# Kernel tuning notes

Measured on AMD Instinct MI355X. Metric: run time of the kernel, lower is better.

## Reference

```python
import jax, jax.numpy as jnp
import numpy as np

B, N, C, NH = 8, 16384, 256, 8
CH = C // NH          # head dim = 32
SCALE = CH ** -0.5
HH = WW = 128         # N = HH*WW
# CoaT crpe window dict {3:2, 5:3, 7:3}: 2 heads->3x3, 3 heads->5x5, 3 heads->7x7


def setup_inputs() -> dict:
    key = jax.random.key(0)
    ks = jax.random.split(key, 9)
    w = lambda k, shp: (jax.random.normal(k, shp, jnp.float32) * 0.02)
    return {
        "x": jax.random.normal(ks[0], (B, N, C), jnp.float32),
        "w_qkv": w(ks[1], (C, 3 * C)),              # qkv_bias=False
        "w_proj": w(ks[2], (C, C)),
        "b_proj": jnp.zeros((C,), jnp.float32),
        "w3": w(ks[3], (3, 3, 1, 2 * CH)),          # HWIO depthwise, 2 heads
        "b3": jnp.zeros((2 * CH,), jnp.float32),
        "w5": w(ks[4], (5, 5, 1, 3 * CH)),          # 3 heads
        "b5": jnp.zeros((3 * CH,), jnp.float32),
        "w7": w(ks[5], (7, 7, 1, 3 * CH)),          # 3 heads
        "b7": jnp.zeros((3 * CH,), jnp.float32),
        "H": HH,
        "W": WW,
    }


def _hydra(q, k, v):
    # q,k,v: [B, h, N, Ch]; normalize over feature dim, O(N) token reduction
    qn = q * jax.lax.rsqrt(jnp.sum(q * q, axis=-1, keepdims=True))
    kn = k * jax.lax.rsqrt(jnp.sum(k * k, axis=-1, keepdims=True))
    kv = jnp.sum(kn * v, axis=-2, keepdims=True)   # [B, h, 1, Ch]
    return qn * kv                                  # broadcast over tokens


def _dwconv(img, kern, bias):
    # img: [B, c, H, W]; kern: [kh, kw, 1, c] (HWIO depthwise)
    c = img.shape[1]
    out = jax.lax.conv_general_dilated(
        img, kern, window_strides=(1, 1), padding="SAME",
        feature_group_count=c,
        dimension_numbers=("NCHW", "HWIO", "NCHW"))
    return out + bias[None, :, None, None]


def _crpe(q, v, Hs, Ws, convs):
    # CoaT ConvRelPosEnc: depthwise conv on v per head group, gated by q
    b, h, n, ch = v.shape
    outs, idx = [], 0
    for heads, kern, bias in convs:
        vs = v[:, idx:idx + heads]                          # [B, hs, N, Ch]
        v_img = vs.transpose(0, 1, 3, 2).reshape(b, heads * ch, Hs, Ws)
        cv = _dwconv(v_img, kern, bias)
        cv = cv.reshape(b, heads, ch, n).transpose(0, 1, 3, 2)
        outs.append(q[:, idx:idx + heads] * cv)
        idx += heads
    return jnp.concatenate(outs, axis=1)                    # [B, h, N, Ch]


def reference(x, w_qkv, w_proj, b_proj, w3, b3, w5, b5, w7, b7, H, W):
    b, n, c = x.shape
    qkv = (x @ w_qkv).reshape(b, n, 3, NH, CH).transpose(2, 0, 3, 1, 4)
    q, k, v = qkv[0], qkv[1], qkv[2]                        # [B, h, N, Ch]
    factor_att = _hydra(q, k, v)
    crpe = _crpe(q, v, H, W, [(2, w3, b3), (3, w5, b5), (3, w7, b7)])
    out = SCALE * factor_att + crpe
    out = out.transpose(0, 2, 1, 3).reshape(b, n, c)        # [B, N, C]
    return out @ w_proj + b_proj
```

## Files before the change

### kernel.cpp

```cpp
#include <hip/hip_runtime.h>
#include <hip/hip_bf16.h>


typedef __hip_bfloat16 bf16;
typedef __bf16 bf16x8 __attribute__((ext_vector_type(8)));
typedef unsigned short u16x8 __attribute__((ext_vector_type(8)));
typedef float f32x4 __attribute__((ext_vector_type(4)));
typedef float f32x8 __attribute__((ext_vector_type(8)));

#define SCALE_ 0.17677669529663687f

__device__ __forceinline__ unsigned short f2b(float f) {
  __hip_bfloat16 h = __float2bfloat16(f);
  return __builtin_bit_cast(unsigned short, h);
}
__device__ __forceinline__ float blo(unsigned u) {
  return __builtin_bit_cast(float, u << 16);
}
__device__ __forceinline__ float bhi(unsigned u) {
  return __builtin_bit_cast(float, u & 0xffff0000u);
}
__device__ __forceinline__ f32x8 unpack8(uint4 u) {
  f32x8 r;
  r[0] = blo(u.x); r[1] = bhi(u.x); r[2] = blo(u.y); r[3] = bhi(u.y);
  r[4] = blo(u.z); r[5] = bhi(u.z); r[6] = blo(u.w); r[7] = bhi(u.w);
  return r;
}
__device__ __forceinline__ uint4 pack8(float a0, float a1, float a2, float a3,
                                       float a4, float a5, float a6, float a7) {
  uint4 s;
  s.x = (unsigned)f2b(a0) | ((unsigned)f2b(a1) << 16);
  s.y = (unsigned)f2b(a2) | ((unsigned)f2b(a3) << 16);
  s.z = (unsigned)f2b(a4) | ((unsigned)f2b(a5) << 16);
  s.w = (unsigned)f2b(a6) | ((unsigned)f2b(a7) << 16);
  return s;
}
__device__ __forceinline__ void gload16(const void* g, void* l) {
  __builtin_amdgcn_global_load_lds(
      (const __attribute__((address_space(1))) unsigned int*)g,
      (__attribute__((address_space(3))) unsigned int*)l, 16, 0, 0);
}
__device__ __forceinline__ f32x4 mfma16(u16x8 a, u16x8 b, f32x4 c) {
  return __builtin_amdgcn_mfma_f32_16x16x32_bf16(
      __builtin_bit_cast(bf16x8, a), __builtin_bit_cast(bf16x8, b), c, 0, 0, 0);
}
__device__ __forceinline__ void barrier_vm4() {
  asm volatile("s_waitcnt vmcnt(4) lgkmcnt(0)" ::: "memory");
  __builtin_amdgcn_s_barrier();
  asm volatile("" ::: "memory");
}
__device__ __forceinline__ void barrier_vm0() {
  asm volatile("s_waitcnt vmcnt(0) lgkmcnt(0)" ::: "memory");
  __builtin_amdgcn_s_barrier();
  asm volatile("" ::: "memory");
}
__device__ __forceinline__ void barrier_vm8() {
  asm volatile("s_waitcnt vmcnt(8) lgkmcnt(0)" ::: "memory");
  __builtin_amdgcn_s_barrier();
  asm volatile("" ::: "memory");
}

__global__ __launch_bounds__(256) void prep_weights(
    const float* __restrict__ wqkv, const float* __restrict__ wproj,
    bf16* __restrict__ wqkvT, bf16* __restrict__ wprojT) {
  const int idx = blockIdx.x * 256 + threadIdx.x;
  if (idx < 768 * 256) {
    const int j = idx >> 8, k = idx & 255;
    wqkvT[idx] = __float2bfloat16(wqkv[k * 768 + j]);
  }
  if (idx < 256 * 256) {
    const int j = idx >> 8, k = idx & 255;
    wprojT[idx] = __float2bfloat16(wproj[k * 256 + j]);
  }
}

__global__ __launch_bounds__(256) void qkv_mfma(
    const float* __restrict__ x, const bf16* __restrict__ wT,
    bf16* __restrict__ qO, bf16* __restrict__ kO, bf16* __restrict__ vO) {
  __shared__ __align__(16) char LDSU[32768];
  char* As = LDSU;
  char* Bs = LDSU + 16384;
  const int tid = threadIdx.x;
  const int l = tid & 63, w = tid >> 6;
  const int wr = w >> 1, wc = w & 1;

  const int lin = blockIdx.y * 6 + blockIdx.x;
  const int xcd = lin & 7, qq = lin >> 3;
  const int jt = qq % 6;
  const int ttile = xcd * 128 + qq / 6;
  const int j0 = jt << 7;
  const int t0 = ttile << 7;

  f32x4 acc[4][4];
#pragma unroll
  for (int m = 0; m < 4; ++m)
#pragma unroll
    for (int t = 0; t < 4; ++t) acc[m][t] = (f32x4){0.f, 0.f, 0.f, 0.f};

  const int arow0 = w * 16 + (l >> 2), arow1 = arow0 + 64;
  const int asl = l & 3;
  const bf16* asrc0 =
      wT + (size_t)(j0 + arow0) * 256 + ((asl ^ ((arow0 >> 1) & 3)) << 3);
  const bf16* asrc1 =
      wT + (size_t)(j0 + arow1) * 256 + ((asl ^ ((arow1 >> 1) & 3)) << 3);
  const int ad0 = w * 1024, ad1 = 4096 + w * 1024;

  const int brow = tid >> 1, bkh = tid & 1;
  const float* xp = x + (size_t)(t0 + brow) * 256 + bkh * 16;
  const int bsw = (brow >> 1) & 3;
  const int bw0 = brow * 64 + (((bkh << 1) ^ bsw) << 4);
  const int bw1 = brow * 64 + ((((bkh << 1) | 1) ^ bsw) << 4);

  const int fr = l & 15;
  const int fq = l >> 4;
  const int fs = (fq ^ ((l >> 1) & 3)) << 4;

  float4 xs[3][4];

  gload16(asrc0, As + ad0);
  gload16(asrc1, As + ad1);
#pragma unroll
  for (int s = 0; s < 3; ++s)
#pragma unroll
    for (int i = 0; i < 4; ++i)
      xs[s][i] = *(const float4*)(xp + s * 32 + i * 4);
  {
    u16x8 p0, p1;
    p0[0] = f2b(xs[0][0].x); p0[1] = f2b(xs[0][0].y);
    p0[2] = f2b(xs[0][0].z); p0[3] = f2b(xs[0][0].w);
    p0[4] = f2b(xs[0][1].x); p0[5] = f2b(xs[0][1].y);
    p0[6] = f2b(xs[0][1].z); p0[7] = f2b(xs[0][1].w);
    p1[0] = f2b(xs[0][2].x); p1[1] = f2b(xs[0][2].y);
    p1[2] = f2b(xs[0][2].z); p1[3] = f2b(xs[0][2].w);
    p1[4] = f2b(xs[0][3].x); p1[5] = f2b(xs[0][3].y);
    p1[6] = f2b(xs[0][3].z); p1[7] = f2b(xs[0][3].w);
    *(u16x8*)(Bs + bw0) = p0;
    *(u16x8*)(Bs + bw1) = p1;
  }
  barrier_vm8();

#pragma unroll
  for (int t = 0; t < 8; ++t) {
    if (t < 7) {
      const int kn = (t + 1) << 5;
      char* Adst = As + (((t + 1) & 1) << 13);
      gload16(asrc0 + kn, Adst + ad0);
      gload16(asrc1 + kn, Adst + ad1);
    }
    if (t < 5) {
#pragma unroll
      for (int i = 0; i < 4; ++i)
        xs[t % 3][i] = *(const float4*)(xp + (t + 3) * 32 + i * 4);
    }
    const char* Ac = As + ((t & 1) << 13);
    const char* Bc = Bs + ((t & 1) << 13);
    u16x8 af[4], bfv[4];
#pragma unroll
    for (int m = 0; m < 4; ++m)
      af[m] = *(const u16x8*)(Ac + (wr * 64 + m * 16 + fr) * 64 + fs);
#pragma unroll
    for (int tt = 0; tt < 4; ++tt)
      bfv[tt] = *(const u16x8*)(Bc + (wc * 64 + tt * 16 + fr) * 64 + fs);
    __builtin_amdgcn_s_setprio(1);
#pragma unroll
    for (int m = 0; m < 4; ++m)
#pragma unroll
      for (int tt = 0; tt < 4; ++tt)
        acc[m][tt] = mfma16(af[m], bfv[tt], acc[m][tt]);
    __builtin_amdgcn_s_setprio(0);
    if (t < 7) {
      const float4* xv = xs[(t + 1) % 3];
      u16x8 p0, p1;
      p0[0] = f2b(xv[0].x); p0[1] = f2b(xv[0].y);
      p0[2] = f2b(xv[0].z); p0[3] = f2b(xv[0].w);
      p0[4] = f2b(xv[1].x); p0[5] = f2b(xv[1].y);
      p0[6] = f2b(xv[1].z); p0[7] = f2b(xv[1].w);
      p1[0] = f2b(xv[2].x); p1[1] = f2b(xv[2].y);
      p1[2] = f2b(xv[2].z); p1[3] = f2b(xv[2].w);
      p1[4] = f2b(xv[3].x); p1[5] = f2b(xv[3].y);
      p1[6] = f2b(xv[3].z); p1[7] = f2b(xv[3].w);
      char* Bdst = Bs + (((t + 1) & 1) << 13);
      *(u16x8*)(Bdst + bw0) = p0;
      *(u16x8*)(Bdst + bw1) = p1;
    }
    if (t < 5) barrier_vm4();
    else if (t < 7) barrier_vm0();
  }
  __syncthreads();

#pragma unroll
  for (int m = 0; m < 4; ++m) {
    const int jq = wr * 16 + m * 4 + fq;
#pragma unroll
    for (int t = 0; t < 4; ++t) {
      const int token = wc * 64 + t * 16 + fr;
      const int p = jq ^ (token & 15);
      uint2 pk;
      pk.x = (unsigned)f2b(acc[m][t][0]) | ((unsigned)f2b(acc[m][t][1]) << 16);
      pk.y = (unsigned)f2b(acc[m][t][2]) | ((unsigned)f2b(acc[m][t][3]) << 16);
      *(uint2*)(LDSU + token * 256 + (p << 3)) = pk;
    }
  }
  __syncthreads();

  const int region = j0 >> 8;
  bf16* outp = (region == 0) ? qO : ((region == 1) ? kO : vO);
  const int b = t0 >> 14;
  const int n0 = t0 & 16383;
  const int jl = j0 & 255;
  const int seg = tid & 15;
#pragma unroll
  for (int r = 0; r < 8; ++r) {
    const int token = r * 16 + (tid >> 4);
    const int tsw = token & 15;
    const uint2 lo = *(const uint2*)(LDSU + token * 256 + (((2 * seg) ^ tsw) << 3));
    const uint2 hi =
        *(const uint2*)(LDSU + token * 256 + (((2 * seg + 1) ^ tsw) << 3));
    uint4 d;
    d.x = lo.x; d.y = lo.y; d.z = hi.x; d.w = hi.y;
    *(uint4*)&outp[((size_t)b * 16384 + n0 + token) * 256 + jl + seg * 8] = d;
  }
}

__global__ __launch_bounds__(256) void kv_reduce(
    const bf16* __restrict__ kT, const bf16* __restrict__ vT,
    float* __restrict__ kv) {
  __shared__ float red[256 * 8];
  const int tid = threadIdx.x;
  const int b = blockIdx.y;
  const int seg = tid & 31;
  f32x8 part = (f32x8)0.f;

  for (int r = 0; r < 32; ++r) {
    const int token = blockIdx.x * 256 + r * 8 + (tid >> 5);
    const size_t roff = ((size_t)b * 16384 + token) * 256;
    const uint4 kd = *(const uint4*)(kT + roff + seg * 8);
    const f32x8 kf = unpack8(kd);
    float ss = 0.f;
#pragma unroll
    for (int i = 0; i < 8; ++i) ss += kf[i] * kf[i];
    ss += __shfl_xor(ss, 1);
    ss += __shfl_xor(ss, 2);
    const float inv = rsqrtf(ss);
    const uint4 vd = *(const uint4*)(vT + roff + seg * 8);
    const f32x8 vf = unpack8(vd);
#pragma unroll
    for (int i = 0; i < 8; ++i) part[i] += kf[i] * inv * vf[i];
  }
#pragma unroll
  for (int i = 0; i < 8; ++i) red[tid * 8 + i] = part[i];
  __syncthreads();
  if (tid < 32) {
    f32x8 s = (f32x8)0.f;
#pragma unroll
    for (int k = 0; k < 8; ++k)
#pragma unroll
      for (int i = 0; i < 8; ++i) s[i] += red[(tid + 32 * k) * 8 + i];
#pragma unroll
    for (int i = 0; i < 8; ++i)
      atomicAdd(&kv[b * 256 + seg * 8 + i], s[i]);
  }
}

#define CRPE_SMEM 37632

template <int K>
__device__ __forceinline__ void crpe_impl(
    char* smem, const bf16* __restrict__ qT, const bf16* __restrict__ vT,
    const float* __restrict__ kvbuf, const float* __restrict__ wp,
    const float* __restrict__ bp, int OC, int hg, int h,
    bf16* __restrict__ mid) {
  constexpr int R = K / 2;
  constexpr int S = 16 + 2 * R;
  constexpr int NSLOT = 4 * ((S - 1) * 23 + 1);
  char* vs = smem;
  float* wlds = (float*)(smem + NSLOT * 16);
  float* blds = wlds + K * K * 32;

  const int tid = threadIdx.x;
  const int tile = blockIdx.y;
  const int b = blockIdx.z;
  const int tx0 = (tile & 7) * 16, ty0 = (tile >> 3) * 16;
  const int px = tid & 15, py = tid >> 4;
  const int ocbase = hg * 32;

  for (int e = tid; e < S * S; e += 256) {
    const int ly = e / S, lx = e - ly * S;
    const int gy = ty0 - R + ly, gx = tx0 - R + lx;
    uint4 d0 = {0, 0, 0, 0}, d1 = {0, 0, 0, 0}, d2 = {0, 0, 0, 0},
          d3 = {0, 0, 0, 0};
    if (gy >= 0 && gy < 128 && gx >= 0 && gx < 128) {
      const uint4* src = (const uint4*)(vT +
          ((size_t)b * 16384 + gy * 128 + gx) * 256 + h * 32);
      d0 = src[0]; d1 = src[1]; d2 = src[2]; d3 = src[3];
    }
    const int p = ly * 22 + lx;
    const int sw = (p >> 1) & 3;
    char* base = vs + ((p << 2) << 4);
    *(uint4*)(base + ((0 ^ sw) << 4)) = d0;
    *(uint4*)(base + ((1 ^ sw) << 4)) = d1;
    *(uint4*)(base + ((2 ^ sw) << 4)) = d2;
    *(uint4*)(base + ((3 ^ sw) << 4)) = d3;
  }
  for (int e = tid; e < K * K * 32; e += 256)
    wlds[e] = wp[(e >> 5) * OC + ocbase + (e & 31)];
  if (tid < 32) blds[tid] = bp[ocbase + tid];
  __syncthreads();

  const float4* bl4 = (const float4*)blds;
  f32x8 acc[4];
#pragma unroll
  for (int cc = 0; cc < 4; ++cc) {
    const float4 b0 = bl4[cc * 2], b1 = bl4[cc * 2 + 1];
    acc[cc][0] = b0.x; acc[cc][1] = b0.y; acc[cc][2] = b0.z; acc[cc][3] = b0.w;
    acc[cc][4] = b1.x; acc[cc][5] = b1.y; acc[cc][6] = b1.z; acc[cc][7] = b1.w;
  }
  const float4* wlds4 = (const float4*)wlds;
#pragma unroll 1
  for (int ky = 0; ky < K; ++ky) {
#pragma unroll
    for (int kx = 0; kx < K; ++kx) {
      const int p = (py + ky) * 22 + (px + kx);
      const int tap = ky * K + kx;
      const int sw = (p >> 1) & 3;
      const char* base = vs + ((p << 2) << 4);
#pragma unroll
      for (int cc = 0; cc < 4; ++cc) {
        const uint4 vv = *(const uint4*)(base + ((cc ^ sw) << 4));
        const f32x8 vf = unpack8(vv);
        const float4 w0 = wlds4[tap * 8 + cc * 2];
        const float4 w1 = wlds4[tap * 8 + cc * 2 + 1];
        acc[cc][0] += vf[0] * w0.x; acc[cc][1] += vf[1] * w0.y;
        acc[cc][2] += vf[2] * w0.z; acc[cc][3] += vf[3] * w0.w;
        acc[cc][4] += vf[4] * w1.x; acc[cc][5] += vf[5] * w1.y;
        acc[cc][6] += vf[6] * w1.z; acc[cc][7] += vf[7] * w1.w;
      }
    }
  }

  const int n = (ty0 + py) * 128 + (tx0 + px);
  const size_t off = ((size_t)b * 16384 + n) * 256 + h * 32;
  const uint4* qsrc = (const uint4*)(qT + off);
  f32x8 qv[4];
  float ss = 0.f;
#pragma unroll
  for (int cc = 0; cc < 4; ++cc) {
    qv[cc] = unpack8(qsrc[cc]);
#pragma unroll
    for (int i = 0; i < 8; ++i) ss += qv[cc][i] * qv[cc][i];
  }
  const float qinv = rsqrtf(ss);
  const float4* kvp = (const float4*)(kvbuf + ((size_t)b * 8 + h) * 32);
  uint4* mdst = (uint4*)(mid + off);
#pragma unroll
  for (int cc = 0; cc < 4; ++cc) {
    const float4 ka = kvp[cc * 2], kb = kvp[cc * 2 + 1];
    float o[8];
    o[0] = SCALE_ * qv[cc][0] * qinv * ka.x + qv[cc][0] * acc[cc][0];
    o[1] = SCALE_ * qv[cc][1] * qinv * ka.y + qv[cc][1] * acc[cc][1];
    o[2] = SCALE_ * qv[cc][2] * qinv * ka.z + qv[cc][2] * acc[cc][2];
    o[3] = SCALE_ * qv[cc][3] * qinv * ka.w + qv[cc][3] * acc[cc][3];
    o[4] = SCALE_ * qv[cc][4] * qinv * kb.x + qv[cc][4] * acc[cc][4];
    o[5] = SCALE_ * qv[cc][5] * qinv * kb.y + qv[cc][5] * acc[cc][5];
    o[6] = SCALE_ * qv[cc][6] * qinv * kb.z + qv[cc][6] * acc[cc][6];
    o[7] = SCALE_ * qv[cc][7] * qinv * kb.w + qv[cc][7] * acc[cc][7];
    mdst[cc] = pack8(o[0], o[1], o[2], o[3], o[4], o[5], o[6], o[7]);
  }
}

__global__ __launch_bounds__(256) void crpe_all(
    const bf16* __restrict__ qT, const bf16* __restrict__ vT,
    const float* __restrict__ kvbuf,
    const float* __restrict__ w3, const float* __restrict__ b3,
    const float* __restrict__ w5, const float* __restrict__ b5,
    const float* __restrict__ w7, const float* __restrict__ b7,
    bf16* __restrict__ mid) {
  __shared__ __align__(16) char smem[CRPE_SMEM];
  const int h = blockIdx.x;
  if (h < 2)
    crpe_impl<3>(smem, qT, vT, kvbuf, w3, b3, 64, h, h, mid);
  else if (h < 5)
    crpe_impl<5>(smem, qT, vT, kvbuf, w5, b5, 96, h - 2, h, mid);
  else
    crpe_impl<7>(smem, qT, vT, kvbuf, w7, b7, 96, h - 5, h, mid);
}

__global__ __launch_bounds__(256) void proj_mfma(
    const bf16* __restrict__ mid, const bf16* __restrict__ wpT,
    const float* __restrict__ bproj, float* __restrict__ out) {
  __shared__ __align__(16) char LDSU[49152];
  char* As = LDSU;
  char* Bs = LDSU + 24576;
  const int tid = threadIdx.x;
  const int l = tid & 63, w = tid >> 6;
  const int wr = w >> 1, wc = w & 1;

  const int lin = blockIdx.y * 2 + blockIdx.x;
  const int xcd = lin & 7, qq = lin >> 3;
  const int jt = qq & 1;
  const int ttile = xcd * 128 + (qq >> 1);
  const int j0 = jt << 7;
  const int tk0 = ttile << 7;

  f32x4 acc[4][4];
#pragma unroll
  for (int m = 0; m < 4; ++m)
#pragma unroll
    for (int t = 0; t < 4; ++t) acc[m][t] = (f32x4){0.f, 0.f, 0.f, 0.f};

  const int row0 = w * 16 + (l >> 2), row1 = row0 + 64;
  const int sl = l & 3;
  const int sw0 = (row0 >> 1) & 3, sw1 = (row1 >> 1) & 3;
  const bf16* asrc0 = wpT + (size_t)(j0 + row0) * 256 + ((sl ^ sw0) << 3);
  const bf16* asrc1 = wpT + (size_t)(j0 + row1) * 256 + ((sl ^ sw1) << 3);
  const bf16* bsrc0 = mid + (size_t)(tk0 + row0) * 256 + ((sl ^ sw0) << 3);
  const bf16* bsrc1 = mid + (size_t)(tk0 + row1) * 256 + ((sl ^ sw1) << 3);
  const int d0 = w * 1024, d1 = 4096 + w * 1024;

  const int fr = l & 15;
  const int fq = l >> 4;
  const int fs = (fq ^ ((l >> 1) & 3)) << 4;

  gload16(asrc0, As + d0);
  gload16(asrc1, As + d1);
  gload16(bsrc0, Bs + d0);
  gload16(bsrc1, Bs + d1);
  gload16(asrc0 + 32, As + 8192 + d0);
  gload16(asrc1 + 32, As + 8192 + d1);
  gload16(bsrc0 + 32, Bs + 8192 + d0);
  gload16(bsrc1 + 32, Bs + 8192 + d1);
  barrier_vm4();

#pragma unroll
  for (int t = 0; t < 8; ++t) {
    if (t < 6) {
      const int kn = (t + 2) << 5;
      const int nb = ((t + 2) % 3) * 8192;
      gload16(asrc0 + kn, As + nb + d0);
      gload16(asrc1 + kn, As + nb + d1);
      gload16(bsrc0 + kn, Bs + nb + d0);
      gload16(bsrc1 + kn, Bs + nb + d1);
    }
    const char* Ac = As + (t % 3) * 8192;
    const char* Bc = Bs + (t % 3) * 8192;
    u16x8 af[4], bfv[4];
#pragma unroll
    for (int m = 0; m < 4; ++m)
      af[m] = *(const u16x8*)(Ac + (wr * 64 + m * 16 + fr) * 64 + fs);
#pragma unroll
    for (int tt = 0; tt < 4; ++tt)
      bfv[tt] = *(const u16x8*)(Bc + (wc * 64 + tt * 16 + fr) * 64 + fs);
    __builtin_amdgcn_s_setprio(1);
#pragma unroll
    for (int m = 0; m < 4; ++m)
#pragma unroll
      for (int tt = 0; tt < 4; ++tt)
        acc[m][tt] = mfma16(af[m], bfv[tt], acc[m][tt]);
    __builtin_amdgcn_s_setprio(0);
    if (t < 6) barrier_vm4();
    else if (t < 7) barrier_vm0();
  }
  __syncthreads();

#pragma unroll
  for (int m = 0; m < 4; ++m) {
    const float4 bias = *(const float4*)&bproj[j0 + wr * 64 + m * 16 + fq * 4];
#pragma unroll
    for (int t = 0; t < 4; ++t) {
      acc[m][t][0] += bias.x;
      acc[m][t][1] += bias.y;
      acc[m][t][2] += bias.z;
      acc[m][t][3] += bias.w;
    }
  }

  for (int chunk = 0; chunk < 2; ++chunk) {
    if (wc == chunk) {
#pragma unroll
      for (int m = 0; m < 4; ++m) {
        const int jq = wr * 16 + m * 4 + fq;
#pragma unroll
        for (int t = 0; t < 4; ++t) {
          const int ltok = t * 16 + fr;
          const int p = jq ^ (ltok & 15);
          float4 r;
          r.x = acc[m][t][0]; r.y = acc[m][t][1];
          r.z = acc[m][t][2]; r.w = acc[m][t][3];
          *(float4*)(LDSU + ltok * 512 + (p << 4)) = r;
        }
      }
    }
    __syncthreads();
    const int seg = tid & 31;
#pragma unroll
    for (int r = 0; r < 8; ++r) {
      const int ltok = r * 8 + (tid >> 5);
      const int p = seg ^ (ltok & 15);
      const float4 dv = *(const float4*)(LDSU + ltok * 512 + (p << 4));
      *(float4*)&out[(size_t)(tk0 + chunk * 64 + ltok) * 256 + j0 + seg * 4] = dv;
    }
    __syncthreads();
  }
}

extern "C" void kernel_launch(void* const* d_in, const int* in_sizes, int n_in,
                              void* d_out, int out_size, void* d_ws,
                              size_t ws_size, hipStream_t stream) {
  const float* x     = (const float*)d_in[0];
  const float* wqkv  = (const float*)d_in[1];
  const float* wproj = (const float*)d_in[2];
  const float* bproj = (const float*)d_in[3];
  const float* w3 = (const float*)d_in[4];
  const float* b3 = (const float*)d_in[5];
  const float* w5 = (const float*)d_in[6];
  const float* b5 = (const float*)d_in[7];
  const float* w7 = (const float*)d_in[8];
  const float* b7 = (const float*)d_in[9];
  float* out = (float*)d_out;

  const size_t PLANE = (size_t)8 * 16384 * 256;
  bf16* qT  = (bf16*)d_ws;
  bf16* vT  = qT + PLANE;
  bf16* kT  = vT + PLANE;
  bf16* mid = kT;
  float* kv = (float*)(kT + PLANE);
  bf16* wqkvT  = (bf16*)(kv + 2048);
  bf16* wprojT = wqkvT + 768 * 256;

  hipMemsetAsync(kv, 0, 2048 * sizeof(float), stream);
  prep_weights<<<dim3(768), 256, 0, stream>>>(wqkv, wproj, wqkvT, wprojT);
  qkv_mfma<<<dim3(6, 1024), 256, 0, stream>>>(x, wqkvT, qT, kT, vT);
  kv_reduce<<<dim3(64, 8), 256, 0, stream>>>(kT, vT, kv);
  crpe_all<<<dim3(8, 64, 8), 256, 0, stream>>>(qT, vT, kv, w3, b3, w5, b5, w7,
                                               b7, mid);
  proj_mfma<<<dim3(2, 1024), 256, 0, stream>>>(mid, wprojT, bproj, out);
}
```

Before: 373.5 us.

## Split CRPE into per-window kernels with 2-pixel register blocking and planar LDS

Replaces the single branching crpe_all kernel with three templated kernels, one per window size. Each thread now computes two horizontally adjacent pixels, so a sliding register reuses each loaded v value across neighbouring taps. The tile becomes 32x16 and LDS is stored as four channel planes with padded rows instead of an XOR swizzle. This is meant to cut LDS reads and unpack work per FMA and to size shared memory per K. It costs three launches instead of one, fewer blocks per kernel, and a channel loop that is no longer unrolled.

```diff
diff --git a/kernel.cpp b/kernel.cpp
--- a/kernel.cpp
+++ b/kernel.cpp
@@ -26,13 +26,12 @@
   r[4] = blo(u.z); r[5] = bhi(u.z); r[6] = blo(u.w); r[7] = bhi(u.w);
   return r;
 }
-__device__ __forceinline__ uint4 pack8(float a0, float a1, float a2, float a3,
-                                       float a4, float a5, float a6, float a7) {
+__device__ __forceinline__ uint4 pack8v(const f32x8 o) {
   uint4 s;
-  s.x = (unsigned)f2b(a0) | ((unsigned)f2b(a1) << 16);
-  s.y = (unsigned)f2b(a2) | ((unsigned)f2b(a3) << 16);
-  s.z = (unsigned)f2b(a4) | ((unsigned)f2b(a5) << 16);
-  s.w = (unsigned)f2b(a6) | ((unsigned)f2b(a7) << 16);
+  s.x = (unsigned)f2b(o[0]) | ((unsigned)f2b(o[1]) << 16);
+  s.y = (unsigned)f2b(o[2]) | ((unsigned)f2b(o[3]) << 16);
+  s.z = (unsigned)f2b(o[4]) | ((unsigned)f2b(o[5]) << 16);
+  s.w = (unsigned)f2b(o[6]) | ((unsigned)f2b(o[7]) << 16);
   return s;
 }
 __device__ __forceinline__ void gload16(const void* g, void* l) {
@@ -58,6 +57,13 @@
   asm volatile("s_waitcnt vmcnt(8) lgkmcnt(0)" ::: "memory");
   __builtin_amdgcn_s_barrier();
   asm volatile("" ::: "memory");
+}
+__device__ __forceinline__ void fma8(f32x8& a, const f32x8 v, const float4 w0,
+                                     const float4 w1) {
+  a[0] += v[0] * w0.x; a[1] += v[1] * w0.y;
+  a[2] += v[2] * w0.z; a[3] += v[3] * w0.w;
+  a[4] += v[4] * w1.x; a[5] += v[5] * w1.y;
+  a[6] += v[6] * w1.z; a[7] += v[7] * w1.w;
 }
 
 __global__ __launch_bounds__(256) void prep_weights(
@@ -262,127 +268,109 @@
   }
 }
 
-#define CRPE_SMEM 37632
-
 template <int K>
-__device__ __forceinline__ void crpe_impl(
-    char* smem, const bf16* __restrict__ qT, const bf16* __restrict__ vT,
+__global__ __launch_bounds__(256) void crpe_conv(
+    const bf16* __restrict__ qT, const bf16* __restrict__ vT,
     const float* __restrict__ kvbuf, const float* __restrict__ wp,
-    const float* __restrict__ bp, int OC, int hg, int h,
+    const float* __restrict__ bp, int OC, int hbase,
     bf16* __restrict__ mid) {
   constexpr int R = K / 2;
-  constexpr int S = 16 + 2 * R;
-  constexpr int NSLOT = 4 * ((S - 1) * 23 + 1);
-  char* vs = smem;
-  float* wlds = (float*)(smem + NSLOT * 16);
-  float* blds = wlds + K * K * 32;
+  constexpr int SY = 16 + 2 * R;
+  constexpr int SXr = 32 + 2 * R;
+  constexpr int SX = SXr + 1;
+  constexpr int PL = SX * SY;
+  __shared__ __align__(16) uint4 vs[4 * PL];
+  __shared__ float wlds[K * K * 32];
+  __shared__ float blds[32];
 
   const int tid = threadIdx.x;
+  const int hg = blockIdx.x;
+  const int h = hbase + hg;
   const int tile = blockIdx.y;
   const int b = blockIdx.z;
-  const int tx0 = (tile & 7) * 16, ty0 = (tile >> 3) * 16;
-  const int px = tid & 15, py = tid >> 4;
+  const int tx0 = (tile & 3) * 32, ty0 = (tile >> 2) * 16;
+  const int tx = tid & 15, ty = tid >> 4;
   const int ocbase = hg * 32;
 
-  for (int e = tid; e < S * S; e += 256) {
-    const int ly = e / S, lx = e - ly * S;
-    const int gy = ty0 - R + ly, gx = tx0 - R + lx;
-    uint4 d0 = {0, 0, 0, 0}, d1 = {0, 0, 0, 0}, d2 = {0, 0, 0, 0},
-          d3 = {0, 0, 0, 0};
-    if (gy >= 0 && gy < 128 && gx >= 0 && gx < 128) {
-      const uint4* src = (const uint4*)(vT +
-          ((size_t)b * 16384 + gy * 128 + gx) * 256 + h * 32);
-      d0 = src[0]; d1 = src[1]; d2 = src[2]; d3 = src[3];
-    }
-    const int p = ly * 22 + lx;
-    const int sw = (p >> 1) & 3;
-    char* base = vs + ((p << 2) << 4);
-    *(uint4*)(base + ((0 ^ sw) << 4)) = d0;
-    *(uint4*)(base + ((1 ^ sw) << 4)) = d1;
-    *(uint4*)(base + ((2 ^ sw) << 4)) = d2;
-    *(uint4*)(base + ((3 ^ sw) << 4)) = d3;
+  {
+    const int cc = tid & 3;
+    for (int e = tid >> 2; e < SXr * SY; e += 64) {
+      const int ly = e / SXr, lx = e - ly * SXr;
+      const int gy = ty0 - R + ly, gx = tx0 - R + lx;
+      uint4 d = {0, 0, 0, 0};
+      if (gy >= 0 && gy < 128 && gx >= 0 && gx < 128)
+        d = *((const uint4*)(vT + ((size_t)b * 16384 + gy * 128 + gx) * 256 +
+                             h * 32) + cc);
+      vs[cc * PL + ly * SX + lx] = d;
+    }
   }
   for (int e = tid; e < K * K * 32; e += 256)
     wlds[e] = wp[(e >> 5) * OC + ocbase + (e & 31)];
   if (tid < 32) blds[tid] = bp[ocbase + tid];
   __syncthreads();
 
+  const int n = (ty0 + ty) * 128 + tx0 + 2 * tx;
+  const size_t off0 = ((size_t)b * 16384 + n) * 256 + h * 32;
+  const uint4* q0 = (const uint4*)(qT + off0);
+  const uint4* q1 = (const uint4*)(qT + off0 + 256);
+  float ss0 = 0.f, ss1 = 0.f;
+#pragma unroll
+  for (int cc = 0; cc < 4; ++cc) {
+    const f32x8 a = unpack8(q0[cc]);
+    const f32x8 c = unpack8(q1[cc]);
+#pragma unroll
+    for (int i = 0; i < 8; ++i) { ss0 += a[i] * a[i]; ss1 += c[i] * c[i]; }
+  }
+  const float qinv0 = rsqrtf(ss0), qinv1 = rsqrtf(ss1);
+  const float4* kvp = (const float4*)(kvbuf + ((size_t)b * 8 + h) * 32);
+  const float4* wlds4 = (const float4*)wlds;
   const float4* bl4 = (const float4*)blds;
-  f32x8 acc[4];
-#pragma unroll
+  uint4* m0 = (uint4*)(mid + off0);
+  uint4* m1 = (uint4*)(mid + off0 + 256);
+
+#pragma unroll 1
   for (int cc = 0; cc < 4; ++cc) {
-    const float4 b0 = bl4[cc * 2], b1 = bl4[cc * 2 + 1];
-    acc[cc][0] = b0.x; acc[cc][1] = b0.y; acc[cc][2] = b0.z; acc[cc][3] = b0.w;
-    acc[cc][4] = b1.x; acc[cc][5] = b1.y; acc[cc][6] = b1.z; acc[cc][7] = b1.w;
-  }
-  const float4* wlds4 = (const float4*)wlds;
-#pragma unroll 1
-  for (int ky = 0; ky < K; ++ky) {
-#pragma unroll
-    for (int kx = 0; kx < K; ++kx) {
-      const int p = (py + ky) * 22 + (px + kx);
-      const int tap = ky * K + kx;
-      const int sw = (p >> 1) & 3;
-      const char* base = vs + ((p << 2) << 4);
-#pragma unroll
-      for (int cc = 0; cc < 4; ++cc) {
-        const uint4 vv = *(const uint4*)(base + ((cc ^ sw) << 4));
-        const f32x8 vf = unpack8(vv);
-        const float4 w0 = wlds4[tap * 8 + cc * 2];
-        const float4 w1 = wlds4[tap * 8 + cc * 2 + 1];
-        acc[cc][0] += vf[0] * w0.x; acc[cc][1] += vf[1] * w0.y;
-        acc[cc][2] += vf[2] * w0.z; acc[cc][3] += vf[3] * w0.w;
-        acc[cc][4] += vf[4] * w1.x; acc[cc][5] += vf[5] * w1.y;
-        acc[cc][6] += vf[6] * w1.z; acc[cc][7] += vf[7] * w1.w;
+    const uint4* vplane = vs + cc * PL;
+    const float4 ba = bl4[cc * 2], bb = bl4[cc * 2 + 1];
+    f32x8 a0, a1;
+    a0[0] = ba.x; a0[1] = ba.y; a0[2] = ba.z; a0[3] = ba.w;
+    a0[4] = bb.x; a0[5] = bb.y; a0[6] = bb.z; a0[7] = bb.w;
+    a1 = a0;
+#pragma unroll
+    for (int ky = 0; ky < K; ++ky) {
+      const uint4* vrow = vplane + (ty + ky) * SX + 2 * tx;
+      f32x8 vcur = unpack8(vrow[0]);
+#pragma unroll
+      for (int kx = 0; kx < K; ++kx) {
+        const f32x8 vnx = unpack8(vrow[kx + 1]);
+        const float4 w0 = wlds4[(ky * K + kx) * 8 + cc * 2];
+        const float4 w1 = wlds4[(ky * K + kx) * 8 + cc * 2 + 1];
+        fma8(a0, vcur, w0, w1);
+        fma8(a1, vnx, w0, w1);
+        vcur = vnx;
       }
     }
-  }
-
-  const int n = (ty0 + py) * 128 + (tx0 + px);
-  const size_t off = ((size_t)b * 16384 + n) * 256 + h * 32;
-  const uint4* qsrc = (const uint4*)(qT + off);
-  f32x8 qv[4];
-  float ss = 0.f;
-#pragma unroll
-  for (int cc = 0; cc < 4; ++cc) {
-    qv[cc] = unpack8(qsrc[cc]);
-#pragma unroll
-    for (int i = 0; i < 8; ++i) ss += qv[cc][i] * qv[cc][i];
-  }
-  const float qinv = rsqrtf(ss);
-  const float4* kvp = (const float4*)(kvbuf + ((size_t)b * 8 + h) * 32);
-  uint4* mdst = (uint4*)(mid + off);
-#pragma unroll
-  for (int cc = 0; cc < 4; ++cc) {
     const float4 ka = kvp[cc * 2], kb = kvp[cc * 2 + 1];
-    float o[8];
-    o[0] = SCALE_ * qv[cc][0] * qinv * ka.x + qv[cc][0] * acc[cc][0];
-    o[1] = SCALE_ * qv[cc][1] * qinv * ka.y + qv[cc][1] * acc[cc][1];
-    o[2] = SCALE_ * qv[cc][2] * qinv * ka.z + qv[cc][2] * acc[cc][2];
-    o[3] = SCALE_ * qv[cc][3] * qinv * ka.w + qv[cc][3] * acc[cc][3];
-    o[4] = SCALE_ * qv[cc][4] * qinv * kb.x + qv[cc][4] * acc[cc][4];
-    o[5] = SCALE_ * qv[cc][5] * qinv * kb.y + qv[cc][5] * acc[cc][5];
-    o[6] = SCALE_ * qv[cc][6] * qinv * kb.z + qv[cc][6] * acc[cc][6];
-    o[7] = SCALE_ * qv[cc][7] * qinv * kb.w + qv[cc][7] * acc[cc][7];
-    mdst[cc] = pack8(o[0], o[1], o[2], o[3], o[4], o[5], o[6], o[7]);
-  }
-}
-
-__global__ __launch_bounds__(256) void crpe_all(
-    const bf16* __restrict__ qT, const bf16* __restrict__ vT,
-    const float* __restrict__ kvbuf,
-    const float* __restrict__ w3, const float* __restrict__ b3,
-    const float* __restrict__ w5, const float* __restrict__ b5,
-    const float* __restrict__ w7, const float* __restrict__ b7,
-    bf16* __restrict__ mid) {
-  __shared__ __align__(16) char smem[CRPE_SMEM];
-  const int h = blockIdx.x;
-  if (h < 2)
-    crpe_impl<3>(smem, qT, vT, kvbuf, w3, b3, 64, h, h, mid);
-  else if (h < 5)
-    crpe_impl<5>(smem, qT, vT, kvbuf, w5, b5, 96, h - 2, h, mid);
-  else
-    crpe_impl<7>(smem, qT, vT, kvbuf, w7, b7, 96, h - 5, h, mid);
+    f32x8 kvf;
+    kvf[0] = ka.x; kvf[1] = ka.y; kvf[2] = ka.z; kvf[3] = ka.w;
+    kvf[4] = kb.x; kvf[5] = kb.y; kvf[6] = kb.z; kvf[7] = kb.w;
+    {
+      const f32x8 qv = unpack8(q0[cc]);
+      f32x8 o;
+#pragma unroll
+      for (int i = 0; i < 8; ++i)
+        o[i] = SCALE_ * qv[i] * qinv0 * kvf[i] + qv[i] * a0[i];
+      m0[cc] = pack8v(o);
+    }
+    {
+      const f32x8 qv = unpack8(q1[cc]);
+      f32x8 o;
+#pragma unroll
+      for (int i = 0; i < 8; ++i)
+        o[i] = SCALE_ * qv[i] * qinv1 * kvf[i] + qv[i] * a1[i];
+      m1[cc] = pack8v(o);
+    }
+  }
 }
 
 __global__ __launch_bounds__(256) void proj_mfma(
@@ -531,7 +519,8 @@
   prep_weights<<<dim3(768), 256, 0, stream>>>(wqkv, wproj, wqkvT, wprojT);
   qkv_mfma<<<dim3(6, 1024), 256, 0, stream>>>(x, wqkvT, qT, kT, vT);
   kv_reduce<<<dim3(64, 8), 256, 0, stream>>>(kT, vT, kv);
-  crpe_all<<<dim3(8, 64, 8), 256, 0, stream>>>(qT, vT, kv, w3, b3, w5, b5, w7,
-                                               b7, mid);
+  crpe_conv<3><<<dim3(2, 32, 8), 256, 0, stream>>>(qT, vT, kv, w3, b3, 64, 0, mid);
+  crpe_conv<5><<<dim3(3, 32, 8), 256, 0, stream>>>(qT, vT, kv, w5, b5, 96, 2, mid);
+  crpe_conv<7><<<dim3(3, 32, 8), 256, 0, stream>>>(qT, vT, kv, w7, b7, 96, 5, mid);
   proj_mfma<<<dim3(2, 1024), 256, 0, stream>>>(mid, wprojT, bproj, out);
 }
```

Result: slower. 381.7 us (+2.2%).
